# Optimization experiments

Hardware: AMD Instinct MI355X
Metric: run time of the kernel (lower is better)

## Reference

```python
import jax, jax.numpy as jnp
import numpy as np

N = 500000
IN_C = 128
OUT_C = 128


def setup_inputs() -> dict:
    key = jax.random.key(0)
    k1, k2, k3, k4 = jax.random.split(key, 4)
    x = jax.random.normal(k1, (N, IN_C), dtype=jnp.float32)
    # E must equal N for the original `out + out[col]` broadcast to be valid
    edge_index = jax.random.randint(k2, (2, N), 0, N, dtype=jnp.int64)
    # Linear(in_channels, out_channels): W [out, in], b [out]
    bound = 1.0 / np.sqrt(IN_C)
    W = jax.random.uniform(k3, (OUT_C, IN_C), dtype=jnp.float32, minval=-bound, maxval=bound)
    b = jax.random.uniform(k4, (OUT_C,), dtype=jnp.float32, minval=-bound, maxval=bound)
    return {"x": x, "edge_index": edge_index, "W": W, "b": b}


def reference(x, edge_index, W, b):
    row, col = edge_index[0], edge_index[1]
    out = x @ W.T + b                      # [N, C] dense projection
    # gather rows by col, then scatter-add +1 at positions row (duplicates accumulate)
    agg = out[col].at[row].add(jnp.float32(1.0))  # [E, C], E == N
    return out + agg
```

## Files before the change

### kernel.cpp

```cpp
#include <hip/hip_runtime.h>
#include <hip/hip_bf16.h>
#include <stdint.h>

typedef __attribute__((ext_vector_type(8))) __bf16 bf16x8;
typedef __attribute__((ext_vector_type(4))) float floatx4;

#define C 128
#define BROWS 64

__device__ __forceinline__ __bf16 f2b(float f) {
  return __builtin_bit_cast(__bf16, __float2bfloat16(f));
}

__global__ void prep_kernel(const int* __restrict__ rowidx, const float* __restrict__ W,
                            int* __restrict__ deg, __bf16* __restrict__ Wb, int n) {
  int i = blockIdx.x * blockDim.x + threadIdx.x;
  if (i < C * C) Wb[i] = f2b(W[i]);
  if (i < n) atomicAdd(deg + rowidx[i], 1);
}

__launch_bounds__(256, 4)
__global__ void gconv_kernel(const float* __restrict__ x,
                             const int* __restrict__ colidx,
                             const __bf16* __restrict__ Wb,
                             const float* __restrict__ bias,
                             const int* __restrict__ deg,
                             float* __restrict__ out, int n) {
  __shared__ bf16x8 sW[2048];

  const int t = threadIdx.x;
  const int lane = t & 63, w = t >> 6;
  const int l15 = lane & 15, quad = lane >> 4;

  const int base = blockIdx.x * BROWS + w * 16;

  int ga  = base + l15;
  int gal = ga < n ? ga : n - 1;
  int cg  = colidx[gal];

  {
    int r = t >> 1, h = t & 1, rx = r & 15;
    const bf16x8* src = (const bf16x8*)(Wb + r * C) + h * 8;
    bf16x8 wreg[8];
#pragma unroll
    for (int i = 0; i < 8; i++) wreg[i] = src[i];
#pragma unroll
    for (int i = 0; i < 8; i++) sW[r * 16 + ((h * 8 + i) ^ rx)] = wreg[i];
  }

  const floatx4* pa = (const floatx4*)(x + (size_t)gal * C) + quad * 2;
  const floatx4* pc = (const floatx4*)(x + (size_t)cg  * C) + quad * 2;
  floatx4 va[8], vc[8];
#pragma unroll
  for (int kc = 0; kc < 4; kc++) {
    va[2 * kc]     = pa[kc * 8];
    va[2 * kc + 1] = pa[kc * 8 + 1];
    vc[2 * kc]     = pc[kc * 8];
    vc[2 * kc + 1] = pc[kc * 8 + 1];
  }

  int gr  = base + quad * 4;
  int grl = (gr + 3 < n) ? gr : ((n - 4) & ~3);
  int4 d4 = *(const int4*)(deg + grl);

  float b2[8];
#pragma unroll
  for (int tt = 0; tt < 8; tt++) b2[tt] = 2.0f * bias[tt * 16 + l15];

  __syncthreads();

  asm volatile("" : "+v"(va[0]), "+v"(va[1]), "+v"(va[2]), "+v"(va[3]),
                    "+v"(va[4]), "+v"(va[5]), "+v"(va[6]), "+v"(va[7]),
                    "+v"(vc[0]), "+v"(vc[1]), "+v"(vc[2]), "+v"(vc[3]),
                    "+v"(vc[4]), "+v"(vc[5]), "+v"(vc[6]), "+v"(vc[7]));

  bf16x8 av[4];
#pragma unroll
  for (int kc = 0; kc < 4; kc++) {
    floatx4 a0 = va[2 * kc], a1 = va[2 * kc + 1];
    floatx4 c0 = vc[2 * kc], c1 = vc[2 * kc + 1];
    av[kc][0] = f2b(a0[0] + c0[0]); av[kc][1] = f2b(a0[1] + c0[1]);
    av[kc][2] = f2b(a0[2] + c0[2]); av[kc][3] = f2b(a0[3] + c0[3]);
    av[kc][4] = f2b(a1[0] + c1[0]); av[kc][5] = f2b(a1[1] + c1[1]);
    av[kc][6] = f2b(a1[2] + c1[2]); av[kc][7] = f2b(a1[3] + c1[3]);
  }

  int sx0 = (quad + 0)  ^ l15;
  int sx1 = (quad + 4)  ^ l15;
  int sx2 = (quad + 8)  ^ l15;
  int sx3 = (quad + 12) ^ l15;

  floatx4 acc[8];
#pragma unroll
  for (int i = 0; i < 8; i++) acc[i] = (floatx4){0.f, 0.f, 0.f, 0.f};

  const bf16x8* wr0 = sW + l15 * 16 + sx0;
  const bf16x8* wr1 = sW + l15 * 16 + sx1;
  const bf16x8* wr2 = sW + l15 * 16 + sx2;
  const bf16x8* wr3 = sW + l15 * 16 + sx3;
#pragma unroll
  for (int tt = 0; tt < 8; tt++) {
    acc[tt] = __builtin_amdgcn_mfma_f32_16x16x32_bf16(av[0], wr0[tt * 256], acc[tt], 0, 0, 0);
    acc[tt] = __builtin_amdgcn_mfma_f32_16x16x32_bf16(av[1], wr1[tt * 256], acc[tt], 0, 0, 0);
    acc[tt] = __builtin_amdgcn_mfma_f32_16x16x32_bf16(av[2], wr2[tt * 256], acc[tt], 0, 0, 0);
    acc[tt] = __builtin_amdgcn_mfma_f32_16x16x32_bf16(av[3], wr3[tt * 256], acc[tt], 0, 0, 0);
  }

  float dvf[4];
  dvf[0] = (float)d4.x; dvf[1] = (float)d4.y;
  dvf[2] = (float)d4.z; dvf[3] = (float)d4.w;
#pragma unroll
  for (int r = 0; r < 4; r++) {
    int g = gr + r;
    if (g < n) {
      float* orow = out + (size_t)g * C + l15;
      float dv = dvf[r];
#pragma unroll
      for (int tt = 0; tt < 8; tt++) orow[tt * 16] = acc[tt][r] + b2[tt] + dv;
    }
  }
}

extern "C" void kernel_launch(void* const* d_in, const int* in_sizes, int n_in,
                              void* d_out, int out_size, void* d_ws, size_t ws_size,
                              hipStream_t stream) {
  const float* x    = (const float*)d_in[0];
  const int*   edge = (const int*)d_in[1];
  const float* W    = (const float*)d_in[2];
  const float* bias = (const float*)d_in[3];
  float* out = (float*)d_out;

  const int n = in_sizes[0] / C;

  int* deg = (int*)d_ws;
  size_t wb_off = ((size_t)n * sizeof(int) + 255) & ~(size_t)255;
  __bf16* Wb = (__bf16*)((char*)d_ws + wb_off);

  hipMemsetAsync(deg, 0, (size_t)n * sizeof(int), stream);

  int nb = (n + 255) / 256;
  prep_kernel<<<nb, 256, 0, stream>>>(edge, W, deg, Wb, n);

  int mb = (n + BROWS - 1) / BROWS;
  gconv_kernel<<<mb, 256, 0, stream>>>(x, edge + n, Wb, bias, deg, out, n);
}
```

Baseline: 504.1 us.

## Use persistent blocks with atomic work-stealing tickets and prefetch next tile indices

Replaces the one-block-per-64-rows grid with a fixed grid of 1280 persistent blocks. Each wavefront grabs 16-row tiles through an atomic ticket counter. The goal is to load W into LDS only once per block and to prefetch the next tile's gather index and degree while the current tile computes. In exchange it adds one global atomic per tile and an extra memset, and the x gathers are no longer issued ahead of the LDS setup barrier.

```diff
diff --git a/kernel.cpp b/kernel.cpp
--- a/kernel.cpp
+++ b/kernel.cpp
@@ -6,7 +6,7 @@
 typedef __attribute__((ext_vector_type(4))) float floatx4;
 
 #define C 128
-#define BROWS 64
+#define TROWS 16
 
 __device__ __forceinline__ __bf16 f2b(float f) {
   return __builtin_bit_cast(__bf16, __float2bfloat16(f));
@@ -19,24 +19,19 @@
   if (i < n) atomicAdd(deg + rowidx[i], 1);
 }
 
-__launch_bounds__(256, 4)
+__launch_bounds__(256, 5)
 __global__ void gconv_kernel(const float* __restrict__ x,
                              const int* __restrict__ colidx,
                              const __bf16* __restrict__ Wb,
                              const float* __restrict__ bias,
                              const int* __restrict__ deg,
+                             int* __restrict__ ticket,
                              float* __restrict__ out, int n) {
   __shared__ bf16x8 sW[2048];
 
   const int t = threadIdx.x;
-  const int lane = t & 63, w = t >> 6;
+  const int lane = t & 63;
   const int l15 = lane & 15, quad = lane >> 4;
-
-  const int base = blockIdx.x * BROWS + w * 16;
-
-  int ga  = base + l15;
-  int gal = ga < n ? ga : n - 1;
-  int cg  = colidx[gal];
 
   {
     int r = t >> 1, h = t & 1, rx = r & 15;
@@ -48,75 +43,90 @@
     for (int i = 0; i < 8; i++) sW[r * 16 + ((h * 8 + i) ^ rx)] = wreg[i];
   }
 
-  const floatx4* pa = (const floatx4*)(x + (size_t)gal * C) + quad * 2;
-  const floatx4* pc = (const floatx4*)(x + (size_t)cg  * C) + quad * 2;
-  floatx4 va[8], vc[8];
-#pragma unroll
-  for (int kc = 0; kc < 4; kc++) {
-    va[2 * kc]     = pa[kc * 8];
-    va[2 * kc + 1] = pa[kc * 8 + 1];
-    vc[2 * kc]     = pc[kc * 8];
-    vc[2 * kc + 1] = pc[kc * 8 + 1];
-  }
-
-  int gr  = base + quad * 4;
-  int grl = (gr + 3 < n) ? gr : ((n - 4) & ~3);
-  int4 d4 = *(const int4*)(deg + grl);
-
   float b2[8];
 #pragma unroll
   for (int tt = 0; tt < 8; tt++) b2[tt] = 2.0f * bias[tt * 16 + l15];
 
+  const int ntk = (n + TROWS - 1) / TROWS;
+
   __syncthreads();
 
-  asm volatile("" : "+v"(va[0]), "+v"(va[1]), "+v"(va[2]), "+v"(va[3]),
-                    "+v"(va[4]), "+v"(va[5]), "+v"(va[6]), "+v"(va[7]),
-                    "+v"(vc[0]), "+v"(vc[1]), "+v"(vc[2]), "+v"(vc[3]),
-                    "+v"(vc[4]), "+v"(vc[5]), "+v"(vc[6]), "+v"(vc[7]));
+  const bf16x8* wr0 = sW + l15 * 16 + ((quad + 0)  ^ l15);
+  const bf16x8* wr1 = sW + l15 * 16 + ((quad + 4)  ^ l15);
+  const bf16x8* wr2 = sW + l15 * 16 + ((quad + 8)  ^ l15);
+  const bf16x8* wr3 = sW + l15 * 16 + ((quad + 12) ^ l15);
 
-  bf16x8 av[4];
+  int tk;
+  if (lane == 0) tk = atomicAdd(ticket, 1);
+  tk = __shfl(tk, 0);
+  {
+    int sb = (tk < ntk ? tk : 0) * TROWS;
+    int ga = sb + l15;          int gal = ga < n ? ga : n - 1;
+    int gr = sb + quad * 4;     int grl = (gr + 3 < n) ? gr : ((n - 4) & ~3);
+    int cg = colidx[gal];
+    int4 d4 = *(const int4*)(deg + grl);
+
+    while (tk < ntk) {
+      const int base = tk * TROWS;
+      int row0 = base + l15; if (row0 >= n) row0 = n - 1;
+
+      const floatx4* pa = (const floatx4*)(x + (size_t)row0 * C) + quad * 2;
+      const floatx4* pc = (const floatx4*)(x + (size_t)cg   * C) + quad * 2;
+      floatx4 va[8], vc[8];
 #pragma unroll
-  for (int kc = 0; kc < 4; kc++) {
-    floatx4 a0 = va[2 * kc], a1 = va[2 * kc + 1];
-    floatx4 c0 = vc[2 * kc], c1 = vc[2 * kc + 1];
-    av[kc][0] = f2b(a0[0] + c0[0]); av[kc][1] = f2b(a0[1] + c0[1]);
-    av[kc][2] = f2b(a0[2] + c0[2]); av[kc][3] = f2b(a0[3] + c0[3]);
-    av[kc][4] = f2b(a1[0] + c1[0]); av[kc][5] = f2b(a1[1] + c1[1]);
-    av[kc][6] = f2b(a1[2] + c1[2]); av[kc][7] = f2b(a1[3] + c1[3]);
-  }
+      for (int kc = 0; kc < 4; kc++) {
+        va[2 * kc]     = pa[kc * 8];
+        va[2 * kc + 1] = pa[kc * 8 + 1];
+        vc[2 * kc]     = pc[kc * 8];
+        vc[2 * kc + 1] = pc[kc * 8 + 1];
+      }
 
-  int sx0 = (quad + 0)  ^ l15;
-  int sx1 = (quad + 4)  ^ l15;
-  int sx2 = (quad + 8)  ^ l15;
-  int sx3 = (quad + 12) ^ l15;
+      int nt;
+      if (lane == 0) nt = atomicAdd(ticket, 1);
+      nt = __shfl(nt, 0);
+      int nsb = (nt < ntk ? nt : 0) * TROWS;
+      int nga = nsb + l15;      int ngal = nga < n ? nga : n - 1;
+      int ngr = nsb + quad * 4; int ngrl = (ngr + 3 < n) ? ngr : ((n - 4) & ~3);
+      int ncg = colidx[ngal];
+      int4 nd4 = *(const int4*)(deg + ngrl);
 
-  floatx4 acc[8];
+      bf16x8 av[4];
 #pragma unroll
-  for (int i = 0; i < 8; i++) acc[i] = (floatx4){0.f, 0.f, 0.f, 0.f};
+      for (int kc = 0; kc < 4; kc++) {
+        floatx4 a0 = va[2 * kc], a1 = va[2 * kc + 1];
+        floatx4 c0 = vc[2 * kc], c1 = vc[2 * kc + 1];
+        av[kc][0] = f2b(a0[0] + c0[0]); av[kc][1] = f2b(a0[1] + c0[1]);
+        av[kc][2] = f2b(a0[2] + c0[2]); av[kc][3] = f2b(a0[3] + c0[3]);
+        av[kc][4] = f2b(a1[0] + c1[0]); av[kc][5] = f2b(a1[1] + c1[1]);
+        av[kc][6] = f2b(a1[2] + c1[2]); av[kc][7] = f2b(a1[3] + c1[3]);
+      }
 
-  const bf16x8* wr0 = sW + l15 * 16 + sx0;
-  const bf16x8* wr1 = sW + l15 * 16 + sx1;
-  const bf16x8* wr2 = sW + l15 * 16 + sx2;
-  const bf16x8* wr3 = sW + l15 * 16 + sx3;
+      floatx4 acc[8];
 #pragma unroll
-  for (int tt = 0; tt < 8; tt++) {
-    acc[tt] = __builtin_amdgcn_mfma_f32_16x16x32_bf16(av[0], wr0[tt * 256], acc[tt], 0, 0, 0);
-    acc[tt] = __builtin_amdgcn_mfma_f32_16x16x32_bf16(av[1], wr1[tt * 256], acc[tt], 0, 0, 0);
-    acc[tt] = __builtin_amdgcn_mfma_f32_16x16x32_bf16(av[2], wr2[tt * 256], acc[tt], 0, 0, 0);
-    acc[tt] = __builtin_amdgcn_mfma_f32_16x16x32_bf16(av[3], wr3[tt * 256], acc[tt], 0, 0, 0);
-  }
+      for (int i = 0; i < 8; i++) acc[i] = (floatx4){0.f, 0.f, 0.f, 0.f};
+#pragma unroll
+      for (int tt = 0; tt < 8; tt++) {
+        acc[tt] = __builtin_amdgcn_mfma_f32_16x16x32_bf16(av[0], wr0[tt * 256], acc[tt], 0, 0, 0);
+        acc[tt] = __builtin_amdgcn_mfma_f32_16x16x32_bf16(av[1], wr1[tt * 256], acc[tt], 0, 0, 0);
+        acc[tt] = __builtin_amdgcn_mfma_f32_16x16x32_bf16(av[2], wr2[tt * 256], acc[tt], 0, 0, 0);
+        acc[tt] = __builtin_amdgcn_mfma_f32_16x16x32_bf16(av[3], wr3[tt * 256], acc[tt], 0, 0, 0);
+      }
 
-  float dvf[4];
-  dvf[0] = (float)d4.x; dvf[1] = (float)d4.y;
-  dvf[2] = (float)d4.z; dvf[3] = (float)d4.w;
+      float dvf[4];
+      dvf[0] = (float)d4.x; dvf[1] = (float)d4.y;
+      dvf[2] = (float)d4.z; dvf[3] = (float)d4.w;
 #pragma unroll
-  for (int r = 0; r < 4; r++) {
-    int g = gr + r;
-    if (g < n) {
-      float* orow = out + (size_t)g * C + l15;
-      float dv = dvf[r];
+      for (int r = 0; r < 4; r++) {
+        int g = gr + r;
+        if (g < n) {
+          float* orow = out + (size_t)g * C + l15;
+          float dv = dvf[r];
 #pragma unroll
-      for (int tt = 0; tt < 8; tt++) orow[tt * 16] = acc[tt][r] + b2[tt] + dv;
+          for (int tt = 0; tt < 8; tt++) orow[tt * 16] = acc[tt][r] + b2[tt] + dv;
+        }
+      }
+
+      tk = nt; cg = ncg; d4 = nd4; gr = ngr;
     }
   }
 }
@@ -135,12 +145,14 @@
   int* deg = (int*)d_ws;
   size_t wb_off = ((size_t)n * sizeof(int) + 255) & ~(size_t)255;
   __bf16* Wb = (__bf16*)((char*)d_ws + wb_off);
+  size_t tk_off = wb_off + (((size_t)C * C * sizeof(__bf16) + 255) & ~(size_t)255);
+  int* ticket = (int*)((char*)d_ws + tk_off);
 
   hipMemsetAsync(deg, 0, (size_t)n * sizeof(int), stream);
+  hipMemsetAsync(ticket, 0, sizeof(int), stream);
 
   int nb = (n + 255) / 256;
   prep_kernel<<<nb, 256, 0, stream>>>(edge, W, deg, Wb, n);
 
-  int mb = (n + BROWS - 1) / BROWS;
-  gconv_kernel<<<mb, 256, 0, stream>>>(x, edge + n, Wb, bias, deg, out, n);
+  gconv_kernel<<<1280, 256, 0, stream>>>(x, edge + n, Wb, bias, deg, ticket, out, n);
 }
```

After: 783.9 us. 55.5% more time.
